# Kernel optimization log

Measured on AMD Instinct MI355X. Metric: run time of the kernel, lower is better.

Reference implementation:

```python
import jax, jax.numpy as jnp
import numpy as np

B = 1024          # number of sessions (graphs)
D = 128           # emb_dim
NH = 4            # num_heads
VOCAB = 50000     # POI vocabulary
NDIST = 512       # distance buckets
MAX_LEN = 160     # max session length


def _lengths():
    # deterministic variable session lengths in [64, 160]
    return np.asarray(64 + (np.arange(B) % 97), dtype=np.int64)


def _layernorm(x, g, b, eps=1e-8):
    mu = x.mean(-1, keepdims=True)
    var = ((x - mu) ** 2).mean(-1, keepdims=True)
    return (x - mu) / jnp.sqrt(var + eps) * g + b


def setup_inputs() -> dict:
    key = jax.random.key(0)
    ks = jax.random.split(key, 16)
    lengths = _lengths()
    N = int(lengths.sum())
    # node -> (graph id, position within graph)
    batch_ids = np.repeat(np.arange(B), lengths)
    node_pos = np.concatenate([np.arange(l) for l in lengths])
    # consecutive (sequence) edges within each session
    starts = np.concatenate([[0], np.cumsum(lengths)[:-1]])
    src = np.concatenate([s + np.arange(l - 1) for s, l in zip(starts, lengths)])
    dst = src + 1
    edge_index = np.stack([src, dst]).astype(np.int64)
    E = edge_index.shape[1]
    s = 1.0 / np.sqrt(D)
    return {
        "POI_embs": jax.random.normal(ks[0], (VOCAB, D), jnp.float32) * 0.02,
        "delta_dis_embs": jax.random.normal(ks[1], (NDIST, D), jnp.float32) * 0.02,
        "att_W": jax.random.normal(ks[2], (D, D), jnp.float32) * s,
        "a_src": jax.random.normal(ks[3], (D,), jnp.float32) * 0.1,
        "a_dst": jax.random.normal(ks[4], (D,), jnp.float32) * 0.1,
        "in_proj_w": jax.random.normal(ks[5], (3 * D, D), jnp.float32) * s,
        "in_proj_b": jnp.zeros((3 * D,), jnp.float32),
        "out_proj_w": jax.random.normal(ks[6], (D, D), jnp.float32) * s,
        "out_proj_b": jnp.zeros((D,), jnp.float32),
        "ln1_g": jnp.ones((D,), jnp.float32), "ln1_b": jnp.zeros((D,), jnp.float32),
        "ln2_g": jnp.ones((D,), jnp.float32), "ln2_b": jnp.zeros((D,), jnp.float32),
        "ffn_w1": jax.random.normal(ks[7], (D, D), jnp.float32) * s,
        "ffn_b1": jnp.zeros((D,), jnp.float32),
        "ffn_w2": jax.random.normal(ks[8], (D, D), jnp.float32) * s,
        "ffn_b2": jnp.zeros((D,), jnp.float32),
        "sess_idx": jax.random.randint(ks[9], (N,), 0, VOCAB),
        "edge_dist": jax.random.randint(ks[10], (E,), 0, NDIST),
        "edge_index": jnp.asarray(edge_index),
        "batch_ids": jnp.asarray(batch_ids),
        "node_pos": jnp.asarray(node_pos),
        "lengths": jnp.asarray(lengths),
    }


def reference(POI_embs, delta_dis_embs, att_W, a_src, a_dst,
              in_proj_w, in_proj_b, out_proj_w, out_proj_b,
              ln1_g, ln1_b, ln2_g, ln2_b,
              ffn_w1, ffn_b1, ffn_w2, ffn_b2,
              sess_idx, edge_dist, edge_index, batch_ids, node_pos, lengths):
    N = sess_idx.shape[0]
    E = edge_index.shape[1]
    # ---- BiSeqGCN: gather -> attention logits -> scatter-softmax -> scatter-add
    x = POI_embs[sess_idx]                    # [N, D] node features
    edge_l = delta_dis_embs[edge_dist]        # [E, D] edge features
    src, dst = edge_index[0], edge_index[1]
    # bidirectional edges: forward (src->dst) then reversed (dst->src)
    j = jnp.concatenate([src, dst])           # message source  x_j
    i = jnp.concatenate([dst, src])           # message target  x_i
    x_i = x[i]                                # [2E, D]
    x_j = x[j]                                # [2E, D]
    fwd_coeff = (x_i[:E] + edge_l) @ att_W.T  # [E, D]
    bwd_coeff = x_i[E:] @ att_W.T             # [E, D]
    logits = jnp.concatenate([fwd_coeff @ a_src, bwd_coeff @ a_dst])  # [2E]
    # scatter-softmax over destination node (torch_geometric softmax, eps=1e-16)
    m = jax.ops.segment_max(logits, i, num_segments=N)
    e = jnp.exp(logits - m[i])
    ssum = jax.ops.segment_sum(e, i, num_segments=N)
    attn = e / (ssum[i] + 1e-16)
    H_u = jax.ops.segment_sum(x_j * attn[:, None], i, num_segments=N)  # [N, D]
    # ---- split/pad to [B, Lmax, D] + padding mask
    Bn = lengths.shape[0]
    pad = jnp.zeros((Bn, MAX_LEN, D), H_u.dtype).at[batch_ids, node_pos].set(H_u)
    mask = jnp.arange(MAX_LEN)[None, :] < lengths[:, None]  # [B, Lmax]
    # ---- MultiheadAttention (Q = LayerNorm(pad); K = V = pad)
    Q = _layernorm(pad, ln1_g, ln1_b)
    Wq, Wk, Wv = jnp.split(in_proj_w, 3, axis=0)
    bq, bk, bv = jnp.split(in_proj_b, 3)
    hd = D // NH
    q = (Q @ Wq.T + bq).reshape(Bn, MAX_LEN, NH, hd)
    k = (pad @ Wk.T + bk).reshape(Bn, MAX_LEN, NH, hd)
    v = (pad @ Wv.T + bv).reshape(Bn, MAX_LEN, NH, hd)
    scores = jnp.einsum('bqhd,bkhd->bhqk', q, k) / jnp.sqrt(jnp.asarray(hd, q.dtype))
    scores = jnp.where(mask[:, None, None, :], scores, -jnp.inf)
    w = jax.nn.softmax(scores, axis=-1)
    ctx = jnp.einsum('bhqk,bkhd->bqhd', w, v).reshape(Bn, MAX_LEN, D)
    out = ctx @ out_proj_w.T + out_proj_b
    out = out + Q
    out = _layernorm(out, ln2_g, ln2_b)
    # ---- PFFN (1x1 convs == per-token linears) with residual
    ffn = jax.nn.relu(out @ ffn_w1.T + ffn_b1) @ ffn_w2.T + ffn_b2
    out = out + ffn
    # ---- masked mean pool over valid positions
    mf = mask[..., None].astype(out.dtype)
    S_u = (out * mf).sum(axis=1) / lengths[:, None].astype(out.dtype)
    return S_u
```

## Files before the change

### kernel.cpp

```cpp
#include <hip/hip_runtime.h>
#include <float.h>


#define D 128
#define NHEAD 4
#define HD 32
#define MAXL 160
#define MAXNK 10
#define VP 168
#define WP 136

typedef __attribute__((ext_vector_type(8))) short short8;
typedef __attribute__((ext_vector_type(4))) float floatx4;

__device__ __forceinline__ float lo2f(unsigned u) {
    union { unsigned i; float f; } x; x.i = u << 16; return x.f;
}
__device__ __forceinline__ float hi2f(unsigned u) {
    union { unsigned i; float f; } x; x.i = u & 0xffff0000u; return x.f;
}
__device__ __forceinline__ unsigned short f2bf(float f) {
    union { float f; unsigned i; } x; x.f = f;
    unsigned r = x.i + 0x7fffu + ((x.i >> 16) & 1u);
    return (unsigned short)(r >> 16);
}
__device__ __forceinline__ unsigned pack2(float a, float b) {
    return (unsigned)f2bf(a) | ((unsigned)f2bf(b) << 16);
}
__device__ __forceinline__ float bf2f(unsigned short u) {
    union { unsigned i; float f; } x; x.i = (unsigned)u << 16; return x.f;
}

__global__ void prep1(const float* __restrict__ att_W, const float* __restrict__ a_src,
                      const float* __restrict__ a_dst, const float* __restrict__ in_proj_w,
                      const float* __restrict__ in_proj_b, const float* __restrict__ g1,
                      const float* __restrict__ b1, float* __restrict__ c_src,
                      float* __restrict__ c_dst, float* __restrict__ u, float* __restrict__ z) {
    int p = threadIdx.x;
    float s = 0.f, d = 0.f, su = 0.f, sz = 0.f;
    for (int q = 0; q < D; q++) {
        float w = att_W[q * D + p];
        s += a_src[q] * w;
        d += a_dst[q] * w;
        float wq = in_proj_w[p * D + q];
        su += g1[q] * wq;
        sz += b1[q] * wq;
    }
    c_src[p] = s;
    c_dst[p] = d;
    u[p] = su;
    z[p] = sz + in_proj_b[p];
}

__global__ void prep2(const float* __restrict__ delta, const float* __restrict__ c_src,
                      const float* __restrict__ in_proj_w, const float* __restrict__ out_proj_w,
                      const float* __restrict__ ffn_w1, const float* __restrict__ ffn_w2,
                      const float* __restrict__ ln1_g, float* __restrict__ tb,
                      unsigned short* __restrict__ wb) {
    int blk = blockIdx.x, t = threadIdx.x;
    if (blk < 128) {
        int b = blk * 4 + (t >> 6);
        int l = t & 63;
        const float* row = delta + (size_t)b * D;
        float s = row[l] * c_src[l] + row[l + 64] * c_src[l + 64];
        #pragma unroll
        for (int o = 32; o; o >>= 1) s += __shfl_down(s, o, 64);
        if (l == 0) tb[b] = s;
    } else {
        int idx = (blk - 128) * 256 + t;
        int m = idx >> 14;
        int within = idx & (D * D - 1);
        float v;
        if (m == 0) v = in_proj_w[within] * ln1_g[within & (D - 1)];
        else if (m == 1) v = in_proj_w[D * D + within];
        else if (m == 2) v = in_proj_w[2 * D * D + within];
        else if (m == 3) v = out_proj_w[within];
        else if (m == 4) v = ffn_w1[within];
        else v = ffn_w2[within];
        wb[idx] = f2bf(v);
    }
}

__launch_bounds__(256)
__global__ void gather_hu(const float* __restrict__ POI, const int* __restrict__ sess_idx,
                          const int* __restrict__ node_pos, const int* __restrict__ batch_ids,
                          const int* __restrict__ edge_dist, const int* __restrict__ lengths,
                          const float* __restrict__ c_src, const float* __restrict__ c_dst,
                          const float* __restrict__ tb, unsigned short* __restrict__ Hu,
                          float* __restrict__ muv, float* __restrict__ rinvv,
                          int* __restrict__ starts, int N) {
    __shared__ unsigned xs[10 * 64];
    __shared__ float s1s[10], s2s[10];
    int R0 = blockIdx.x * 8;
    int t = threadIdx.x;
    int hw = t >> 5, l32 = t & 31;
    float4 cs4 = *(const float4*)(c_src + l32 * 4);
    float4 cd4 = *(const float4*)(c_dst + l32 * 4);
    #pragma unroll
    for (int i = hw; i < 10; i += 8) {
        int n = R0 - 1 + i;
        if (n >= 0 && n < N) {
            int row = sess_idx[n];
            float4 v = *(const float4*)(POI + (size_t)row * D + l32 * 4);
            ((uint2*)(xs + i * 64))[l32] = make_uint2(pack2(v.x, v.y), pack2(v.z, v.w));
            if (i >= 1 && i <= 8) {
                float ps = v.x * cs4.x + v.y * cs4.y + v.z * cs4.z + v.w * cs4.w;
                float pd = v.x * cd4.x + v.y * cd4.y + v.z * cd4.z + v.w * cd4.w;
                #pragma unroll
                for (int o = 16; o; o >>= 1) {
                    ps += __shfl_down(ps, o, 64);
                    pd += __shfl_down(pd, o, 64);
                }
                if (l32 == 0) { s1s[i] = ps; s2s[i] = pd; }
            }
        }
    }
    __syncthreads();
    int j = hw;
    int n = R0 + j;
    if (n >= N) return;
    int g = batch_ids[n], pos = node_pos[n], L = lengths[g];
    bool hasF = pos > 0;
    bool hasB = pos < L - 1;
    float la = hasF ? (s1s[j + 1] + tb[edge_dist[n - 1 - g]]) : -FLT_MAX;
    float lb = hasB ? s2s[j + 1] : -FLT_MAX;
    float m = fmaxf(la, lb);
    float ea = hasF ? __expf(la - m) : 0.f;
    float eb = hasB ? __expf(lb - m) : 0.f;
    float inv = 1.f / (ea + eb + 1e-16f);
    float wa = ea * inv, wb = eb * inv;
    uint2 a = hasF ? ((const uint2*)(xs + j * 64))[l32] : make_uint2(0u, 0u);
    uint2 b = hasB ? ((const uint2*)(xs + (j + 2) * 64))[l32] : make_uint2(0u, 0u);
    float h0 = wa * lo2f(a.x) + wb * lo2f(b.x);
    float h1 = wa * hi2f(a.x) + wb * hi2f(b.x);
    float h2 = wa * lo2f(a.y) + wb * lo2f(b.y);
    float h3 = wa * hi2f(a.y) + wb * hi2f(b.y);
    ((uint2*)Hu)[(size_t)n * 32 + l32] = make_uint2(pack2(h0, h1), pack2(h2, h3));
    float s = h0 + h1 + h2 + h3;
    float ss = h0 * h0 + h1 * h1 + h2 * h2 + h3 * h3;
    #pragma unroll
    for (int o = 1; o < 32; o <<= 1) {
        s += __shfl_xor(s, o, 64);
        ss += __shfl_xor(ss, o, 64);
    }
    if (l32 == 0) {
        float mu = s * (1.f / D);
        float var = ss * (1.f / D) - mu * mu;
        muv[n] = mu;
        rinvv[n] = rsqrtf(var + 1e-8f);
        if (pos == 0) starts[g] = n;
    }
}

__launch_bounds__(256)
__global__ void qkv_split(const unsigned short* __restrict__ Hu, const unsigned short* __restrict__ wb,
                          const float* __restrict__ in_proj_b, const float* __restrict__ u,
                          const float* __restrict__ z, const float* __restrict__ muv,
                          const float* __restrict__ rinvv,
                          unsigned short* __restrict__ qo, unsigned short* __restrict__ ko,
                          unsigned short* __restrict__ vT, int M, int Npad) {
    __shared__ unsigned short Wl[128 * WP];
    int t = threadIdx.x;
    int wv = t >> 6, lane = t & 63;
    int quad = lane >> 4, l16 = lane & 15;
    int r0 = blockIdx.x * 128;
    int rbase = r0 + wv * 32;
    int p = blockIdx.y;
    const float ASCALE = 0.25504364148122793f;
    const unsigned short* W = wb + (p == 0 ? 1 : p == 1 ? 2 : 0) * (D * D);
    for (int i = t; i < 2048; i += 256) {
        int c = i >> 4, kc = (i & 15) * 8;
        *(uint4*)&Wl[c * WP + kc] = *(const uint4*)(W + c * 128 + kc);
    }
    short8 af[2][4];
    #pragma unroll
    for (int mt = 0; mt < 2; mt++) {
        int r = rbase + mt * 16 + l16;
        #pragma unroll
        for (int kk = 0; kk < 4; kk++) {
            if (r < M) af[mt][kk] = *(const short8*)(Hu + (size_t)r * D + kk * 32 + quad * 8);
            else af[mt][kk] = (short8){0, 0, 0, 0, 0, 0, 0, 0};
        }
    }
    __syncthreads();
    floatx4 acc[2][8];
    #pragma unroll
    for (int i = 0; i < 2; i++)
        #pragma unroll
        for (int j = 0; j < 8; j++) acc[i][j] = (floatx4){0.f, 0.f, 0.f, 0.f};
    #pragma unroll
    for (int kk = 0; kk < 4; kk++)
        #pragma unroll
        for (int nt = 0; nt < 8; nt++) {
            short8 bf = *(const short8*)&Wl[(nt * 16 + l16) * WP + kk * 32 + quad * 8];
            acc[0][nt] = __builtin_amdgcn_mfma_f32_16x16x32_bf16(af[0][kk], bf, acc[0][nt], 0, 0, 0);
            acc[1][nt] = __builtin_amdgcn_mfma_f32_16x16x32_bf16(af[1][kk], bf, acc[1][nt], 0, 0, 0);
        }
    __syncthreads();
    if (p == 1) {
        #pragma unroll
        for (int nt = 0; nt < 8; nt++) {
            int col = nt * 16 + l16;
            float bv = in_proj_b[2 * D + col];
            #pragma unroll
            for (int mt = 0; mt < 2; mt++)
                #pragma unroll
                for (int r = 0; r < 4; r++) {
                    int ln = wv * 32 + mt * 16 + quad * 4 + r;
                    Wl[col * WP + ln] = (r0 + ln < M) ? f2bf(acc[mt][nt][r] + bv)
                                                      : (unsigned short)0;
                }
        }
    } else if (p == 0) {
        #pragma unroll
        for (int nt = 0; nt < 8; nt++) {
            int col = nt * 16 + l16;
            float bv = in_proj_b[D + col];
            #pragma unroll
            for (int mt = 0; mt < 2; mt++)
                #pragma unroll
                for (int r = 0; r < 4; r++)
                    Wl[(wv * 32 + mt * 16 + quad * 4 + r) * WP + col] =
                        f2bf(acc[mt][nt][r] + bv);
        }
    } else {
        float uc[8], zc[8];
        #pragma unroll
        for (int nt = 0; nt < 8; nt++) {
            uc[nt] = u[nt * 16 + l16];
            zc[nt] = z[nt * 16 + l16] * ASCALE;
        }
        #pragma unroll
        for (int mt = 0; mt < 2; mt++)
            #pragma unroll
            for (int r = 0; r < 4; r++) {
                int ln = wv * 32 + mt * 16 + quad * 4 + r;
                int grow = r0 + ln;
                float mr = grow < M ? muv[grow] : 0.f;
                float rr = (grow < M ? rinvv[grow] : 0.f) * ASCALE;
                #pragma unroll
                for (int nt = 0; nt < 8; nt++)
                    Wl[ln * WP + nt * 16 + l16] =
                        f2bf(rr * (acc[mt][nt][r] - mr * uc[nt]) + zc[nt]);
            }
    }
    __syncthreads();
    if (p == 1) {
        for (int i = t; i < 2048; i += 256) {
            int col = i >> 4, c8 = (i & 15) * 8;
            *(uint4*)(vT + (size_t)col * Npad + r0 + c8) = *(uint4*)&Wl[col * WP + c8];
        }
    } else {
        unsigned short* out = (p == 0) ? ko : qo;
        for (int i = t; i < 2048; i += 256) {
            int row = i >> 4, c8 = (i & 15) * 8;
            if (r0 + row < M)
                *(uint4*)(out + (size_t)(r0 + row) * D + c8) = *(uint4*)&Wl[row * WP + c8];
        }
    }
}

__launch_bounds__(128)
__global__ void attn9(const unsigned short* __restrict__ qb,
                      const unsigned short* __restrict__ kb,
                      const unsigned short* __restrict__ vT,
                      const int* __restrict__ starts, const int* __restrict__ lengths,
                      unsigned short* __restrict__ ctx, int Npad) {
    __shared__ unsigned short Vt[HD * VP];
    __shared__ unsigned short Pb[2 * 16 * VP];
    int g = blockIdx.x;
    if (gridDim.x == 1024) {
        int bid = blockIdx.x;
        if (bid < 430) { int r = 96 - bid / 10; g = r + 97 * (bid % 10); }
        else { int b2 = bid - 430; int r = 53 - b2 / 11; g = r + 97 * (b2 % 11); }
    }
    int h = blockIdx.y;
    int start = starts[g], L = lengths[g];
    int t = threadIdx.x;
    int wv = t >> 6, lane = t & 63;
    int l16 = lane & 15, quad = lane >> 4;
    int nk = (L + 15) >> 4;
    int nk2 = (L + 31) >> 5;
    for (int i = t; i < 16 * VP; i += 128) ((unsigned*)Pb)[i] = 0u;
    int nch = nk2 * 4;
    for (int i = t; i < HD * nch; i += 128) {
        int r = i / nch, c = i - r * nch;
        *(uint4*)&Vt[r * VP + c * 8] =
            *(const uint4*)(vT + (size_t)(h * HD + r) * Npad + start + c * 8);
    }
    short8 kf[MAXNK];
    #pragma unroll
    for (int kt = 0; kt < MAXNK; kt++) {
        kf[kt] = (short8){0, 0, 0, 0, 0, 0, 0, 0};
        if (kt < nk) {
            int r = kt * 16 + l16;
            if (r < L) kf[kt] = *(const short8*)(kb + (size_t)(start + r) * D + h * HD + quad * 8);
        }
    }
    short8 qf[5];
    #pragma unroll
    for (int i = 0; i < 5; i++) {
        qf[i] = (short8){0, 0, 0, 0, 0, 0, 0, 0};
        int qt = wv + 2 * i;
        if (qt < nk) {
            int qrow = qt * 16 + l16;
            if (qrow < L)
                qf[i] = *(const short8*)(qb + (size_t)(start + qrow) * D + h * HD + quad * 8);
        }
    }
    __syncthreads();
    unsigned short* Pw = Pb + wv * 16 * VP;
    #pragma unroll
    for (int i = 0; i < 5; i++) {
        int qt = wv + 2 * i;
        if (qt >= nk) break;
        int q0 = qt * 16;
        floatx4 sacc[MAXNK];
        #pragma unroll
        for (int kt = 0; kt < MAXNK; kt++)
            if (kt < nk)
                sacc[kt] = __builtin_amdgcn_mfma_f32_16x16x32_bf16(
                    kf[kt], qf[i], (floatx4){0.f, 0.f, 0.f, 0.f}, 0, 0, 0);
        float lsum = 0.f;
        #pragma unroll
        for (int kt = 0; kt < MAXNK; kt++)
            if (kt < nk) {
                #pragma unroll
                for (int r = 0; r < 4; r++) {
                    int key = kt * 16 + quad * 4 + r;
                    float p = (key < L) ? __builtin_amdgcn_exp2f(sacc[kt][r]) : 0.f;
                    sacc[kt][r] = p;
                    lsum += p;
                }
            }
        #pragma unroll
        for (int kt = 0; kt < MAXNK; kt++)
            if (kt < nk) {
                *(unsigned*)&Pw[l16 * VP + kt * 16 + quad * 4] =
                    pack2(sacc[kt][0], sacc[kt][1]);
                *(unsigned*)&Pw[l16 * VP + kt * 16 + quad * 4 + 2] =
                    pack2(sacc[kt][2], sacc[kt][3]);
            }
        lsum += __shfl_xor(lsum, 16);
        lsum += __shfl_xor(lsum, 32);
        float inv = 1.f / lsum;
        #pragma unroll
        for (int nc = 0; nc < 2; nc++) {
            floatx4 oacc = (floatx4){0.f, 0.f, 0.f, 0.f};
            #pragma unroll
            for (int kc = 0; kc < 5; kc++)
                if (kc < nk2) {
                    short8 pf = *(const short8*)&Pw[l16 * VP + kc * 32 + quad * 8];
                    short8 vf = *(const short8*)&Vt[(nc * 16 + l16) * VP + kc * 32 + quad * 8];
                    oacc = __builtin_amdgcn_mfma_f32_16x16x32_bf16(pf, vf, oacc, 0, 0, 0);
                }
            #pragma unroll
            for (int r = 0; r < 4; r++) {
                int qr = q0 + quad * 4 + r;
                if (qr < L)
                    ctx[(size_t)(start + qr) * D + h * HD + nc * 16 + l16] =
                        f2bf(oacc[r] * inv);
            }
        }
    }
}

__launch_bounds__(256)
__global__ void outproj_ln2(const unsigned short* __restrict__ ctx, const unsigned short* __restrict__ W,
                            const float* __restrict__ bo, const unsigned short* __restrict__ Hu,
                            const float* __restrict__ muv, const float* __restrict__ rinvv,
                            const float* __restrict__ g1, const float* __restrict__ b1,
                            const float* __restrict__ g2, const float* __restrict__ b2,
                            unsigned short* __restrict__ out, int M) {
    __shared__ unsigned short Wl[128 * WP];
    int t = threadIdx.x;
    int wv = t >> 6, lane = t & 63;
    int quad = lane >> 4, l16 = lane & 15;
    int r0 = blockIdx.x * 128;
    int rbase = r0 + wv * 32;
    for (int i = t; i < 2048; i += 256) {
        int c = i >> 4, kc = (i & 15) * 8;
        *(uint4*)&Wl[c * WP + kc] = *(const uint4*)(W + c * 128 + kc);
    }
    __syncthreads();
    floatx4 acc[2][8];
    #pragma unroll
    for (int i = 0; i < 2; i++)
        #pragma unroll
        for (int j = 0; j < 8; j++) acc[i][j] = (floatx4){0.f, 0.f, 0.f, 0.f};
    #pragma unroll
    for (int kk = 0; kk < 4; kk++) {
        short8 af[2];
        #pragma unroll
        for (int mt = 0; mt < 2; mt++) {
            int r = rbase + mt * 16 + l16;
            if (r < M) af[mt] = *(const short8*)(ctx + (size_t)r * D + kk * 32 + quad * 8);
            else af[mt] = (short8){0, 0, 0, 0, 0, 0, 0, 0};
        }
        #pragma unroll
        for (int nt = 0; nt < 8; nt++) {
            short8 bf = *(const short8*)&Wl[(nt * 16 + l16) * WP + kk * 32 + quad * 8];
            acc[0][nt] = __builtin_amdgcn_mfma_f32_16x16x32_bf16(af[0], bf, acc[0][nt], 0, 0, 0);
            acc[1][nt] = __builtin_amdgcn_mfma_f32_16x16x32_bf16(af[1], bf, acc[1][nt], 0, 0, 0);
        }
    }
    __syncthreads();
    for (int i = t; i < 2048; i += 256) {
        int row = i >> 4, c8 = (i & 15) * 8;
        uint4 hv = make_uint4(0u, 0u, 0u, 0u);
        if (r0 + row < M) hv = *(const uint4*)(Hu + (size_t)(r0 + row) * D + c8);
        *(uint4*)&Wl[row * WP + c8] = hv;
    }
    __syncthreads();
    float g1c[8], b1c[8], boc[8], g2c[8], b2c[8];
    #pragma unroll
    for (int nt = 0; nt < 8; nt++) {
        int col = nt * 16 + l16;
        g1c[nt] = g1[col]; b1c[nt] = b1[col]; boc[nt] = bo[col];
        g2c[nt] = g2[col]; b2c[nt] = b2[col];
    }
    #pragma unroll
    for (int mt = 0; mt < 2; mt++) {
        #pragma unroll
        for (int r = 0; r < 4; r++) {
            int lrow = wv * 32 + mt * 16 + quad * 4 + r;
            int grow = r0 + lrow;
            bool ok = grow < M;
            float mr = ok ? muv[grow] : 0.f;
            float rr = ok ? rinvv[grow] : 0.f;
            float vv[8];
            float s = 0.f, ss = 0.f;
            #pragma unroll
            for (int nt = 0; nt < 8; nt++) {
                float huv = bf2f(Wl[lrow * WP + nt * 16 + l16]);
                float qv = (huv - mr) * rr * g1c[nt] + b1c[nt];
                float v = acc[mt][nt][r] + boc[nt] + qv;
                vv[nt] = v;
                s += v; ss += v * v;
            }
            #pragma unroll
            for (int o = 1; o < 16; o <<= 1) {
                s += __shfl_xor(s, o, 64);
                ss += __shfl_xor(ss, o, 64);
            }
            float mu = s * (1.f / D);
            float var = ss * (1.f / D) - mu * mu;
            float rinv = rsqrtf(var + 1e-8f);
            #pragma unroll
            for (int nt = 0; nt < 8; nt++)
                Wl[lrow * WP + nt * 16 + l16] =
                    f2bf((vv[nt] - mu) * rinv * g2c[nt] + b2c[nt]);
        }
    }
    __syncthreads();
    for (int i = t; i < 2048; i += 256) {
        int row = i >> 4, c8 = (i & 15) * 8;
        if (r0 + row < M)
            *(uint4*)(out + (size_t)(r0 + row) * D + c8) = *(uint4*)&Wl[row * WP + c8];
    }
}

__launch_bounds__(256)
__global__ void ffn_fused(const unsigned short* __restrict__ out2, const unsigned short* __restrict__ W1,
                          const float* __restrict__ b1f, const unsigned short* __restrict__ W2,
                          const float* __restrict__ b2f, unsigned short* __restrict__ fin, int M) {
    __shared__ unsigned short Wl[128 * WP];
    int t = threadIdx.x;
    int wv = t >> 6, lane = t & 63;
    int quad = lane >> 4, l16 = lane & 15;
    int r0 = blockIdx.x * 128;
    int rbase = r0 + wv * 32;
    int lbase = wv * 32;
    for (int i = t; i < 2048; i += 256) {
        int c = i >> 4, kc = (i & 15) * 8;
        *(uint4*)&Wl[c * WP + kc] = *(const uint4*)(W1 + c * 128 + kc);
    }
    short8 af[2][4];
    #pragma unroll
    for (int mt = 0; mt < 2; mt++) {
        int r = rbase + mt * 16 + l16;
        #pragma unroll
        for (int kk = 0; kk < 4; kk++) {
            if (r < M) af[mt][kk] = *(const short8*)(out2 + (size_t)r * D + kk * 32 + quad * 8);
            else af[mt][kk] = (short8){0, 0, 0, 0, 0, 0, 0, 0};
        }
    }
    __syncthreads();
    floatx4 acc[2][8];
    #pragma unroll
    for (int i = 0; i < 2; i++)
        #pragma unroll
        for (int j = 0; j < 8; j++) acc[i][j] = (floatx4){0.f, 0.f, 0.f, 0.f};
    #pragma unroll
    for (int kk = 0; kk < 4; kk++)
        #pragma unroll
        for (int nt = 0; nt < 8; nt++) {
            short8 bf = *(const short8*)&Wl[(nt * 16 + l16) * WP + kk * 32 + quad * 8];
            acc[0][nt] = __builtin_amdgcn_mfma_f32_16x16x32_bf16(af[0][kk], bf, acc[0][nt], 0, 0, 0);
            acc[1][nt] = __builtin_amdgcn_mfma_f32_16x16x32_bf16(af[1][kk], bf, acc[1][nt], 0, 0, 0);
        }
    __syncthreads();
    #pragma unroll
    for (int nt = 0; nt < 8; nt++) {
        int col = nt * 16 + l16;
        float bv = b1f[col];
        #pragma unroll
        for (int mt = 0; mt < 2; mt++)
            #pragma unroll
            for (int r = 0; r < 4; r++)
                Wl[(lbase + mt * 16 + quad * 4 + r) * WP + col] =
                    f2bf(fmaxf(acc[mt][nt][r] + bv, 0.f));
    }
    __syncthreads();
    short8 af2[2][4];
    #pragma unroll
    for (int mt = 0; mt < 2; mt++)
        #pragma unroll
        for (int kk = 0; kk < 4; kk++)
            af2[mt][kk] = *(const short8*)&Wl[(lbase + mt * 16 + l16) * WP + kk * 32 + quad * 8];
    __syncthreads();
    for (int i = t; i < 2048; i += 256) {
        int c = i >> 4, kc = (i & 15) * 8;
        *(uint4*)&Wl[c * WP + kc] = *(const uint4*)(W2 + c * 128 + kc);
    }
    __syncthreads();
    #pragma unroll
    for (int i = 0; i < 2; i++)
        #pragma unroll
        for (int j = 0; j < 8; j++) acc[i][j] = (floatx4){0.f, 0.f, 0.f, 0.f};
    #pragma unroll
    for (int kk = 0; kk < 4; kk++)
        #pragma unroll
        for (int nt = 0; nt < 8; nt++) {
            short8 bf = *(const short8*)&Wl[(nt * 16 + l16) * WP + kk * 32 + quad * 8];
            acc[0][nt] = __builtin_amdgcn_mfma_f32_16x16x32_bf16(af2[0][kk], bf, acc[0][nt], 0, 0, 0);
            acc[1][nt] = __builtin_amdgcn_mfma_f32_16x16x32_bf16(af2[1][kk], bf, acc[1][nt], 0, 0, 0);
        }
    __syncthreads();
    #pragma unroll
    for (int nt = 0; nt < 8; nt++) {
        int col = nt * 16 + l16;
        float bv = b2f[col];
        #pragma unroll
        for (int mt = 0; mt < 2; mt++)
            #pragma unroll
            for (int r = 0; r < 4; r++)
                Wl[(lbase + mt * 16 + quad * 4 + r) * WP + col] = f2bf(acc[mt][nt][r] + bv);
    }
    __syncthreads();
    for (int i = t; i < 2048; i += 256) {
        int row = i >> 4, c8 = (i & 15) * 8;
        int grow = r0 + row;
        if (grow < M) {
            uint4 a = *(uint4*)&Wl[row * WP + c8];
            uint4 b = *(const uint4*)(out2 + (size_t)grow * D + c8);
            uint4 o;
            o.x = pack2(lo2f(a.x) + lo2f(b.x), hi2f(a.x) + hi2f(b.x));
            o.y = pack2(lo2f(a.y) + lo2f(b.y), hi2f(a.y) + hi2f(b.y));
            o.z = pack2(lo2f(a.z) + lo2f(b.z), hi2f(a.z) + hi2f(b.z));
            o.w = pack2(lo2f(a.w) + lo2f(b.w), hi2f(a.w) + hi2f(b.w));
            *(uint4*)(fin + (size_t)grow * D + c8) = o;
        }
    }
}

__launch_bounds__(512)
__global__ void pool_k(const unsigned short* __restrict__ fin, const int* __restrict__ starts,
                       const int* __restrict__ lengths, float* __restrict__ out) {
    __shared__ float ps[4][128];
    int g = blockIdx.x;
    int t = threadIdx.x;
    int d = t & 127, qt = t >> 7;
    int start = starts[g], L = lengths[g];
    int qlen = (L + 3) >> 2;
    int p0 = qt * qlen;
    int p1 = min(L, p0 + qlen);
    float s0 = 0.f, s1 = 0.f, s2 = 0.f, s3 = 0.f;
    int p = p0;
    for (; p + 4 <= p1; p += 4) {
        s0 += bf2f(fin[(size_t)(start + p) * D + d]);
        s1 += bf2f(fin[(size_t)(start + p + 1) * D + d]);
        s2 += bf2f(fin[(size_t)(start + p + 2) * D + d]);
        s3 += bf2f(fin[(size_t)(start + p + 3) * D + d]);
    }
    for (; p < p1; p++) s0 += bf2f(fin[(size_t)(start + p) * D + d]);
    ps[qt][d] = (s0 + s1) + (s2 + s3);
    __syncthreads();
    if (qt == 0)
        out[(size_t)g * D + d] =
            ((ps[0][d] + ps[1][d]) + (ps[2][d] + ps[3][d])) / (float)L;
}

extern "C" void kernel_launch(void* const* d_in, const int* in_sizes, int n_in,
                              void* d_out, int out_size, void* d_ws, size_t ws_size,
                              hipStream_t stream) {
    const float* POI        = (const float*)d_in[0];
    const float* delta      = (const float*)d_in[1];
    const float* att_W      = (const float*)d_in[2];
    const float* a_src      = (const float*)d_in[3];
    const float* a_dst      = (const float*)d_in[4];
    const float* in_proj_w  = (const float*)d_in[5];
    const float* in_proj_b  = (const float*)d_in[6];
    const float* out_proj_w = (const float*)d_in[7];
    const float* out_proj_b = (const float*)d_in[8];
    const float* ln1_g      = (const float*)d_in[9];
    const float* ln1_b      = (const float*)d_in[10];
    const float* ln2_g      = (const float*)d_in[11];
    const float* ln2_b      = (const float*)d_in[12];
    const float* ffn_w1     = (const float*)d_in[13];
    const float* ffn_b1     = (const float*)d_in[14];
    const float* ffn_w2     = (const float*)d_in[15];
    const float* ffn_b2     = (const float*)d_in[16];
    const int* sess_idx     = (const int*)d_in[17];
    const int* edge_dist    = (const int*)d_in[18];
    const int* batch_ids    = (const int*)d_in[20];
    const int* node_pos     = (const int*)d_in[21];
    const int* lengths      = (const int*)d_in[22];

    int N = in_sizes[17];
    int B = in_sizes[22];
    int gb = (N + 127) / 128;
    int Npad = gb * 128;

    char* base = (char*)d_ws;
    size_t off = 0;
    auto alloc = [&](size_t bytes) { size_t c = off; off = (off + bytes + 255) & ~(size_t)255; return c; };
    size_t o_csrc  = alloc(D * 4);
    size_t o_cdst  = alloc(D * 4);
    size_t o_t     = alloc(512 * 4);
    size_t o_start = alloc((size_t)B * 4);
    size_t o_mu    = alloc((size_t)N * 4);
    size_t o_ri    = alloc((size_t)N * 4);
    size_t o_u     = alloc(D * 4);
    size_t o_z     = alloc(D * 4);
    size_t o_wb    = alloc(6 * D * D * 2);
    size_t nb      = (size_t)Npad * D * 2;
    size_t o_A = alloc(nb);
    size_t o_B = alloc(nb);
    size_t o_C = alloc(nb);
    size_t o_D = alloc(nb);
    if (ws_size < off) return;

    float* c_src = (float*)(base + o_csrc);
    float* c_dst = (float*)(base + o_cdst);
    float* tb    = (float*)(base + o_t);
    int*   starts = (int*)(base + o_start);
    float* muv   = (float*)(base + o_mu);
    float* rinvv = (float*)(base + o_ri);
    float* u     = (float*)(base + o_u);
    float* z     = (float*)(base + o_z);
    unsigned short* wb = (unsigned short*)(base + o_wb);
    unsigned short* bufA = (unsigned short*)(base + o_A);
    unsigned short* bufB = (unsigned short*)(base + o_B);
    unsigned short* bufC = (unsigned short*)(base + o_C);
    unsigned short* bufD = (unsigned short*)(base + o_D);

    prep1<<<1, 128, 0, stream>>>(att_W, a_src, a_dst, in_proj_w, in_proj_b,
                                 ln1_g, ln1_b, c_src, c_dst, u, z);
    prep2<<<512, 256, 0, stream>>>(delta, c_src, in_proj_w, out_proj_w,
                                   ffn_w1, ffn_w2, ln1_g, tb, wb);
    gather_hu<<<(N + 7) / 8, 256, 0, stream>>>(POI, sess_idx, node_pos, batch_ids,
                                               edge_dist, lengths, c_src, c_dst, tb,
                                               bufB, muv, rinvv, starts, N);

    qkv_split<<<dim3(gb, 3), 256, 0, stream>>>(bufB, wb, in_proj_b, u, z, muv, rinvv,
                                               bufC, bufD, bufA, N, Npad);

    attn9<<<dim3(B, NHEAD), 128, 0, stream>>>(bufC, bufD, bufA, starts, lengths, bufC, Npad);

    outproj_ln2<<<gb, 256, 0, stream>>>(bufC, wb + 3 * D * D, out_proj_b, bufB, muv, rinvv,
                                        ln1_g, ln1_b, ln2_g, ln2_b, bufD, N);
    ffn_fused<<<gb, 256, 0, stream>>>(bufD, wb + 4 * D * D, ffn_b1, wb + 5 * D * D, ffn_b2,
                                      bufA, N);
    pool_k<<<B, 512, 0, stream>>>(bufA, starts, lengths, (float*)d_out);
}
```

Measured before the change: 316.6 us.

## Use hardware bf16 pack, fold key mask into MFMA init, trim P zeroing

Replaces the software round-to-nearest bf16 conversion with the v_cvt_pk_bf16_f32 instruction and writes packed pairs in the V-transpose store. In attention, the key-length mask is folded into the MFMA accumulator init as a large negative bias, so exp2 yields zero without a per-element compare. Zeroing of the P buffer is reduced to the single padding tile that only odd nk needs, and P stores are merged into 64-bit writes. This cuts ALU and LDS work, at the cost of relying on exp2 of -3e38 flushing to zero and on hardware rounding semantics.

```diff
diff --git a/kernel.cpp b/kernel.cpp
--- a/kernel.cpp
+++ b/kernel.cpp
@@ -19,13 +19,13 @@
 __device__ __forceinline__ float hi2f(unsigned u) {
     union { unsigned i; float f; } x; x.i = u & 0xffff0000u; return x.f;
 }
+__device__ __forceinline__ unsigned pack2(float a, float b) {
+    unsigned r;
+    asm("v_cvt_pk_bf16_f32 %0, %1, %2" : "=v"(r) : "v"(a), "v"(b));
+    return r;
+}
 __device__ __forceinline__ unsigned short f2bf(float f) {
-    union { float f; unsigned i; } x; x.f = f;
-    unsigned r = x.i + 0x7fffu + ((x.i >> 16) & 1u);
-    return (unsigned short)(r >> 16);
-}
-__device__ __forceinline__ unsigned pack2(float a, float b) {
-    return (unsigned)f2bf(a) | ((unsigned)f2bf(b) << 16);
+    return (unsigned short)pack2(f, 0.f);
 }
 __device__ __forceinline__ float bf2f(unsigned short u) {
     union { unsigned i; float f; } x; x.i = (unsigned)u << 16; return x.f;
@@ -205,10 +205,11 @@
             #pragma unroll
             for (int mt = 0; mt < 2; mt++)
                 #pragma unroll
-                for (int r = 0; r < 4; r++) {
+                for (int r = 0; r < 4; r += 2) {
                     int ln = wv * 32 + mt * 16 + quad * 4 + r;
-                    Wl[col * WP + ln] = (r0 + ln < M) ? f2bf(acc[mt][nt][r] + bv)
-                                                      : (unsigned short)0;
+                    float v0 = (r0 + ln     < M) ? acc[mt][nt][r]     + bv : 0.f;
+                    float v1 = (r0 + ln + 1 < M) ? acc[mt][nt][r + 1] + bv : 0.f;
+                    *(unsigned*)&Wl[col * WP + ln] = pack2(v0, v1);
                 }
         }
     } else if (p == 0) {
@@ -281,7 +282,13 @@
     int l16 = lane & 15, quad = lane >> 4;
     int nk = (L + 15) >> 4;
     int nk2 = (L + 31) >> 5;
-    for (int i = t; i < 16 * VP; i += 128) ((unsigned*)Pb)[i] = 0u;
+    unsigned short* Pw = Pb + wv * 16 * VP;
+    if (nk & 1) {
+        for (int i = lane; i < 128; i += 64) {
+            int row = i >> 3, c = i & 7;
+            ((unsigned*)(Pw + row * VP + nk * 16))[c] = 0u;
+        }
+    }
     int nch = nk2 * 4;
     for (int i = t; i < HD * nch; i += 128) {
         int r = i / nch, c = i - r * nch;
@@ -308,8 +315,13 @@
                 qf[i] = *(const short8*)(qb + (size_t)(start + qrow) * D + h * HD + quad * 8);
         }
     }
-    __syncthreads();
-    unsigned short* Pw = Pb + wv * 16 * VP;
+    floatx4 cinit[MAXNK];
+    #pragma unroll
+    for (int kt = 0; kt < MAXNK; kt++)
+        #pragma unroll
+        for (int r = 0; r < 4; r++)
+            cinit[kt][r] = (kt * 16 + quad * 4 + r < L) ? 0.f : -3.0e38f;
+    __syncthreads();
     #pragma unroll
     for (int i = 0; i < 5; i++) {
         int qt = wv + 2 * i;
@@ -320,26 +332,20 @@
         for (int kt = 0; kt < MAXNK; kt++)
             if (kt < nk)
                 sacc[kt] = __builtin_amdgcn_mfma_f32_16x16x32_bf16(
-                    kf[kt], qf[i], (floatx4){0.f, 0.f, 0.f, 0.f}, 0, 0, 0);
+                    kf[kt], qf[i], cinit[kt], 0, 0, 0);
         float lsum = 0.f;
         #pragma unroll
         for (int kt = 0; kt < MAXNK; kt++)
             if (kt < nk) {
                 #pragma unroll
                 for (int r = 0; r < 4; r++) {
-                    int key = kt * 16 + quad * 4 + r;
-                    float p = (key < L) ? __builtin_amdgcn_exp2f(sacc[kt][r]) : 0.f;
+                    float p = __builtin_amdgcn_exp2f(sacc[kt][r]);
                     sacc[kt][r] = p;
                     lsum += p;
                 }
-            }
-        #pragma unroll
-        for (int kt = 0; kt < MAXNK; kt++)
-            if (kt < nk) {
-                *(unsigned*)&Pw[l16 * VP + kt * 16 + quad * 4] =
-                    pack2(sacc[kt][0], sacc[kt][1]);
-                *(unsigned*)&Pw[l16 * VP + kt * 16 + quad * 4 + 2] =
-                    pack2(sacc[kt][2], sacc[kt][3]);
+                *(uint2*)&Pw[l16 * VP + kt * 16 + quad * 4] =
+                    make_uint2(pack2(sacc[kt][0], sacc[kt][1]),
+                               pack2(sacc[kt][2], sacc[kt][3]));
             }
         lsum += __shfl_xor(lsum, 16);
         lsum += __shfl_xor(lsum, 32);
```

After: 316.3 us. About the same (-0.1%).
